# Kernel tuning notes

Measured on AMD Instinct MI355X. Metric: run time of the kernel, lower is better.

Reference implementation:

```python
import jax, jax.numpy as jnp
import numpy as np

B, T, E, H, V = 4, 2048, 1024, 16, 32000
HD = E // H  # head_dim = 64


def setup_inputs() -> dict:
    key = jax.random.key(0)
    ks = jax.random.split(key, 16)
    s = 0.02
    p = lambda k, shp: jax.random.normal(k, shp, jnp.float32) * s
    return {
        "x": jax.random.randint(ks[0], (B, T), 0, V),
        "tok_emb": p(ks[1], (V, E)),
        "pos_emb": p(ks[2], (T, E)),
        "m_Wq": p(ks[3], (E, E)), "m_Wk": p(ks[4], (E, E)),
        "m_Wv": p(ks[5], (E, E)), "m_Wo": p(ks[6], (E, E)),
        "m_bo": jnp.zeros((E,), jnp.float32),
        "h_Wq": p(ks[7], (E, E)), "h_Wk": p(ks[8], (E, E)),
        "h_Wv": p(ks[9], (E, E)), "h_Wo": p(ks[10], (E, E)),
        "h_bo": jnp.zeros((E,), jnp.float32),
        "f_W1": p(ks[11], (E, 512)), "f_b1": jnp.zeros((512,), jnp.float32),
        "f_W2": p(ks[12], (512, 1024)), "f_b2": jnp.zeros((1024,), jnp.float32),
        "f_W3": p(ks[13], (1024, 512)), "f_b3": jnp.zeros((512,), jnp.float32),
        "f_W4": p(ks[14], (512, E)), "f_b4": jnp.zeros((E,), jnp.float32),
        "ln_g": jnp.ones((E,), jnp.float32),
        "ln_b": jnp.zeros((E,), jnp.float32),
    }


def _layernorm(x, g, b, eps=1e-5):
    m = x.mean(-1, keepdims=True)
    v = ((x - m) ** 2).mean(-1, keepdims=True)
    return (x - m) / jnp.sqrt(v + eps) * g + b


def _mha(x, Wq, Wk, Wv, Wo, bo, masked):
    b, t, e = x.shape
    # [b, t, e] -> [b, h, t, hd]
    q = (x @ Wq).reshape(b, t, H, HD).transpose(0, 2, 1, 3)
    k = (x @ Wk).reshape(b, t, H, HD).transpose(0, 2, 1, 3)
    v = (x @ Wv).reshape(b, t, H, HD).transpose(0, 2, 1, 3)
    wei = jnp.einsum("bhqd,bhkd->bhqk", q, k) / np.float32(np.sqrt(HD))
    if masked:  # causal (module is in training mode by default)
        causal = jnp.tril(jnp.ones((t, t), dtype=bool))
        wei = jnp.where(causal, wei, -jnp.inf)
    att = jax.nn.softmax(wei, axis=-1)
    out = jnp.einsum("bhqk,bhkd->bhqd", att, v).transpose(0, 2, 1, 3).reshape(b, t, e)
    return out @ Wo + bo


def _ffn(x, W1, b1, W2, b2, W3, b3, W4, b4):
    h = jax.nn.relu(x @ W1 + b1)
    h = jax.nn.relu(h @ W2 + b2)
    h = jax.nn.relu(h @ W3 + b3)
    return h @ W4 + b4


def reference(x, tok_emb, pos_emb,
              m_Wq, m_Wk, m_Wv, m_Wo, m_bo,
              h_Wq, h_Wk, h_Wv, h_Wo, h_bo,
              f_W1, f_b1, f_W2, f_b2, f_W3, f_b3, f_W4, f_b4,
              ln_g, ln_b):
    e = tok_emb[x] + pos_emb[jnp.arange(x.shape[1])]          # [B, T, E]
    r = _layernorm(e + _mha(e, m_Wq, m_Wk, m_Wv, m_Wo, m_bo, True), ln_g, ln_b)
    r = _layernorm(r + _mha(r, h_Wq, h_Wk, h_Wv, h_Wo, h_bo, False), ln_g, ln_b)
    r = _layernorm(r + _ffn(r, f_W1, f_b1, f_W2, f_b2, f_W3, f_b3, f_W4, f_b4), ln_g, ln_b)
    return r
```

## Files before the change

kernel.cpp:

```cpp
#include <hip/hip_runtime.h>
#include <hip/hip_bf16.h>


typedef __attribute__((ext_vector_type(8))) short v8s;
typedef __attribute__((ext_vector_type(4))) short v4s;
typedef __attribute__((ext_vector_type(4))) float v4f;
typedef __attribute__((ext_vector_type(4))) unsigned int v4u;

#define MFMA16(a, b, c) __builtin_amdgcn_mfma_f32_16x16x32_bf16((a), (b), (c), 0, 0, 0)

typedef const __attribute__((address_space(1))) void* gas1_t;
typedef __attribute__((address_space(3))) void* las3_t;

__device__ __forceinline__ void gl_lds16(const void* g, void* l) {
  __builtin_amdgcn_global_load_lds((gas1_t)g, (las3_t)l, 16, 0, 0);
}

__device__ __forceinline__ unsigned short f2bf(float f) {
  __hip_bfloat16 h = __float2bfloat16(f);
  return *reinterpret_cast<unsigned short*>(&h);
}

__device__ __forceinline__ float bf2f(unsigned short u) {
  union { unsigned int i; float f; } v;
  v.i = (unsigned int)u << 16;
  return v.f;
}

__device__ __forceinline__ float fast_exp2(float x) {
  float r;
  asm("v_exp_f32 %0, %1" : "=v"(r) : "v"(x));
  return r;
}

__device__ __forceinline__ unsigned int cvt_pk_bf16(float lo, float hi) {
  unsigned int r;
  asm("v_cvt_pk_bf16_f32 %0, %1, %2" : "=v"(r) : "v"(lo), "v"(hi));
  return r;
}

__device__ __forceinline__ float max3f(float a, float b, float c) {
  float r;
  asm("v_max3_f32 %0, %1, %2, %3" : "=v"(r) : "v"(a), "v"(b), "v"(c));
  return r;
}

#define QSCALE 0.18033688011112042f

__global__ __launch_bounds__(256)
void transpose_bf16(const float* __restrict__ src, unsigned short* __restrict__ dst,
                    int K, int N) {
  __shared__ float tile[32][33];
  const int n0 = blockIdx.x * 32, k0 = blockIdx.y * 32;
  const int tx = threadIdx.x & 31, ty = threadIdx.x >> 5;
#pragma unroll
  for (int i = 0; i < 32; i += 8)
    tile[ty + i][tx] = src[(size_t)(k0 + ty + i) * N + n0 + tx];
  __syncthreads();
#pragma unroll
  for (int i = 0; i < 32; i += 8)
    dst[(size_t)(n0 + ty + i) * K + k0 + tx] = f2bf(tile[tx][ty + i]);
}

__global__ __launch_bounds__(256)
void embed_k(const int* __restrict__ x, const float* __restrict__ tok,
             const float* __restrict__ pos, unsigned short* __restrict__ act) {
  const int t = blockIdx.x, tid = threadIdx.x;
  const int id = x[t], tp = t & 2047;
  float4 v = ((const float4*)(tok + (size_t)id * 1024))[tid];
  float4 p = ((const float4*)(pos + (size_t)tp * 1024))[tid];
  ushort4 u;
  u.x = f2bf(v.x + p.x); u.y = f2bf(v.y + p.y);
  u.z = f2bf(v.z + p.z); u.w = f2bf(v.w + p.w);
  ((ushort4*)(act + (size_t)t * 1024))[tid] = u;
}

__global__ __launch_bounds__(256)
void gemm_bt(const unsigned short* __restrict__ A, const unsigned short* __restrict__ Bt,
             const float* __restrict__ bias, void* __restrict__ C,
             int M, int N, int K, int flags) {
  __shared__ __align__(16) unsigned short As[128 * 64];
  __shared__ __align__(16) unsigned short Bs[128 * 64];
  const int tid = threadIdx.x;
  const int w = tid >> 6, l = tid & 63;
  const int lr = l & 15, lg = l >> 4;
  const int wm = w & 1, wn = w >> 1;
  const int m0 = blockIdx.x * 128, n0 = blockIdx.y * 128;
  const int ra = l >> 3, ka = (l & 7) * 8;

  v4f acc[4][4];
  const v4f vzero = {0.f, 0.f, 0.f, 0.f};
#pragma unroll
  for (int m = 0; m < 4; ++m)
#pragma unroll
    for (int n = 0; n < 4; ++n) acc[m][n] = vzero;

  for (int k0 = 0; k0 < K; k0 += 64) {
#pragma unroll
    for (int i = 0; i < 4; ++i) {
      const int c = w + i * 4;
      gl_lds16(A  + (size_t)(m0 + c * 8 + ra) * K + k0 + ka, &As[c * 512]);
      gl_lds16(Bt + (size_t)(n0 + c * 8 + ra) * K + k0 + ka, &Bs[c * 512]);
    }
    __syncthreads();
#pragma unroll
    for (int kk = 0; kk < 2; ++kk) {
      v8s af[4], bb[4];
#pragma unroll
      for (int m = 0; m < 4; ++m)
        af[m] = *(const v8s*)&As[(wm * 64 + m * 16 + lr) * 64 + kk * 32 + lg * 8];
#pragma unroll
      for (int n = 0; n < 4; ++n)
        bb[n] = *(const v8s*)&Bs[(wn * 64 + n * 16 + lr) * 64 + kk * 32 + lg * 8];
#pragma unroll
      for (int m = 0; m < 4; ++m)
#pragma unroll
        for (int n = 0; n < 4; ++n)
          acc[m][n] = MFMA16(af[m], bb[n], acc[m][n]);
    }
    __syncthreads();
  }

  const bool relu = flags & 1, obf = flags & 2, qs = flags & 4;
#pragma unroll
  for (int n = 0; n < 4; ++n) {
    const int col = n0 + wn * 64 + n * 16 + lr;
    const float bv = bias ? bias[col] : 0.f;
    const float sc = (qs && col < 1024) ? QSCALE : 1.f;
#pragma unroll
    for (int m = 0; m < 4; ++m) {
      const int row = m0 + wm * 64 + m * 16 + lg * 4;
#pragma unroll
      for (int r = 0; r < 4; ++r) {
        float v = (acc[m][n][r] + bv) * sc;
        if (relu) v = fmaxf(v, 0.f);
        if (obf) ((unsigned short*)C)[(size_t)(row + r) * N + col] = f2bf(v);
        else     ((float*)C)[(size_t)(row + r) * N + col] = v;
      }
    }
  }
}

#define LDQ 3072
template <bool CAUSAL>
__global__ __launch_bounds__(512)
void flash_attn(const unsigned short* __restrict__ qkv, unsigned short* __restrict__ O) {
  __shared__ __align__(16) unsigned short Kt[64 * 64];
  __shared__ __align__(16) unsigned short Vt[64 * 64];
  const int tid = threadIdx.x;
  const int w = tid >> 6, l = tid & 63, lr = l & 15, lg = l >> 4;
  const int b = blockIdx.y >> 4, h = blockIdx.y & 15;
  const size_t baseq = ((size_t)b * 2048) * LDQ + h * 64;
  const size_t baseo = ((size_t)b * 2048) * 1024 + h * 64;
  const int kswz = (lr & 7) * 8;
  const int vswz = lr * 4;

  const int kra = l >> 3, kka = ((l & 7) ^ (l >> 3)) * 8;
  const int vp_ = tid & 31, vd0 = ((tid >> 5) & 7) * 8;

  const int nq = CAUSAL ? 2 : 1;
  for (int qi = 0; qi < nq; ++qi) {
    const int qt = CAUSAL ? (qi ? 15 - (int)blockIdx.x : (int)blockIdx.x)
                          : (int)blockIdx.x;
    const int q0w = qt * 128 + w * 16;

    const unsigned short* qp = qkv + baseq + (size_t)(q0w + lr) * LDQ + lg * 8;
    const v8s qf0 = *(const v8s*)qp;
    const v8s qf1 = *(const v8s*)(qp + 32);

    v4f acc[4];
    const v4f vzero = {0.f, 0.f, 0.f, 0.f};
#pragma unroll
    for (int n = 0; n < 4; ++n) acc[n] = vzero;
    float mrow = -INFINITY, lrow = 0.f;

    const int kv_end = CAUSAL ? qt * 128 + 128 : 2048;
    for (int kv0 = 0; kv0 < kv_end; kv0 += 64) {
      if (w >= 4) {
#pragma unroll
        for (int i = 0; i < 2; ++i) {
          const int c = (w - 4) * 2 + i;
          gl_lds16(qkv + baseq + 1024 + (size_t)(kv0 + c * 8 + kra) * LDQ + kka,
                   &Kt[c * 512]);
        }
      } else {
        const unsigned short* va = qkv + baseq + 2048 + (size_t)(kv0 + 2 * vp_) * LDQ + vd0;
        const v8s v0 = *(const v8s*)va;
        const v8s v1 = *(const v8s*)(va + LDQ);
#pragma unroll
        for (int j = 0; j < 8; ++j) {
          const unsigned int pk = (unsigned int)(unsigned short)v0[j] |
                                  ((unsigned int)(unsigned short)v1[j] << 16);
          *(unsigned int*)&Vt[(vd0 + j) * 64 + ((2 * vp_) ^ (((vd0 + j) & 15) * 4))] = pk;
        }
      }
      __syncthreads();

      v4f s[4];
#pragma unroll
      for (int n = 0; n < 4; ++n) s[n] = vzero;
      __builtin_amdgcn_s_setprio(1);
#pragma unroll
      for (int kk = 0; kk < 2; ++kk) {
#pragma unroll
        for (int n = 0; n < 4; ++n) {
          const v8s kf = *(const v8s*)&Kt[(n * 16 + lr) * 64 + ((kk * 32 + lg * 8) ^ kswz)];
          s[n] = MFMA16(kf, kk ? qf1 : qf0, s[n]);
        }
      }
      __builtin_amdgcn_s_setprio(0);

      if (CAUSAL && (kv0 + 63 > q0w)) {
        const int qg = q0w + lr;
#pragma unroll
        for (int n = 0; n < 4; ++n) {
          const int kvb = kv0 + n * 16 + lg * 4;
#pragma unroll
          for (int r = 0; r < 4; ++r)
            if (kvb + r > qg) s[n][r] = -INFINITY;
        }
      }

      float tm;
      {
        const float t0 = max3f(s[0][0], s[0][1], s[0][2]);
        const float t1 = max3f(s[0][3], s[1][0], s[1][1]);
        const float t2 = max3f(s[1][2], s[1][3], s[2][0]);
        const float t3 = max3f(s[2][1], s[2][2], s[2][3]);
        const float t4 = max3f(s[3][0], s[3][1], s[3][2]);
        tm = max3f(t0, t1, s[3][3]);
        tm = max3f(tm, t2, t3);
        tm = fmaxf(tm, t4);
      }
      tm = fmaxf(tm, __shfl_xor(tm, 16));
      tm = fmaxf(tm, __shfl_xor(tm, 32));

      if (__any(tm > mrow + 8.f)) {
        const float mn = fmaxf(mrow, tm);
        const float fac = fast_exp2(mrow - mn);
        mrow = mn;
        lrow *= fac;
        float facT[4];
#pragma unroll
        for (int r = 0; r < 4; ++r)
          facT[r] = __shfl(fac, (l & 48) | (lg * 4 + r));
#pragma unroll
        for (int n = 0; n < 4; ++n)
#pragma unroll
          for (int r = 0; r < 4; ++r) acc[n][r] *= facT[r];
      }

      float rs = 0.f;
#pragma unroll
      for (int n = 0; n < 4; ++n)
#pragma unroll
        for (int r = 0; r < 4; ++r) {
          s[n][r] = fast_exp2(s[n][r] - mrow);
          rs += s[n][r];
        }
      rs += __shfl_xor(rs, 16);
      rs += __shfl_xor(rs, 32);
      lrow += rs;

      v4u pu0, pu1;
      pu0.x = cvt_pk_bf16(s[0][0], s[0][1]); pu0.y = cvt_pk_bf16(s[0][2], s[0][3]);
      pu0.z = cvt_pk_bf16(s[1][0], s[1][1]); pu0.w = cvt_pk_bf16(s[1][2], s[1][3]);
      pu1.x = cvt_pk_bf16(s[2][0], s[2][1]); pu1.y = cvt_pk_bf16(s[2][2], s[2][3]);
      pu1.z = cvt_pk_bf16(s[3][0], s[3][1]); pu1.w = cvt_pk_bf16(s[3][2], s[3][3]);
      v8s pf0, pf1;
      __builtin_memcpy(&pf0, &pu0, 16);
      __builtin_memcpy(&pf1, &pu1, 16);

      __builtin_amdgcn_s_setprio(1);
#pragma unroll
      for (int kk = 0; kk < 2; ++kk) {
#pragma unroll
        for (int n = 0; n < 4; ++n) {
          const int rowb = (n * 16 + lr) * 64;
          const v4s va_ = *(const v4s*)&Vt[rowb + ((kk * 32 + lg * 4) ^ vswz)];
          const v4s vb_ = *(const v4s*)&Vt[rowb + ((kk * 32 + 16 + lg * 4) ^ vswz)];
          const v8s vf = __builtin_shufflevector(va_, vb_, 0, 1, 2, 3, 4, 5, 6, 7);
          acc[n] = MFMA16(kk ? pf1 : pf0, vf, acc[n]);
        }
      }
      __builtin_amdgcn_s_setprio(0);
      __syncthreads();
    }

    float lT[4];
#pragma unroll
    for (int r = 0; r < 4; ++r)
      lT[r] = __shfl(lrow, (l & 48) | (lg * 4 + r));
#pragma unroll
    for (int n = 0; n < 4; ++n)
#pragma unroll
      for (int r = 0; r < 4; ++r) {
        const float v = acc[n][r] / lT[r];
        O[baseo + (size_t)(q0w + lg * 4 + r) * 1024 + n * 16 + lr] = f2bf(v);
      }
  }
}

__global__ __launch_bounds__(256)
void add_ln(const unsigned short* __restrict__ ra, const unsigned short* __restrict__ rb,
            const float* __restrict__ g, const float* __restrict__ be,
            unsigned short* __restrict__ ob, float* __restrict__ of) {
  const int t = blockIdx.x, tid = threadIdx.x;
  const ushort4 ua = ((const ushort4*)(ra + (size_t)t * 1024))[tid];
  const ushort4 ub = ((const ushort4*)(rb + (size_t)t * 1024))[tid];
  float4 s;
  s.x = bf2f(ua.x) + bf2f(ub.x);
  s.y = bf2f(ua.y) + bf2f(ub.y);
  s.z = bf2f(ua.z) + bf2f(ub.z);
  s.w = bf2f(ua.w) + bf2f(ub.w);
  float sum = s.x + s.y + s.z + s.w;
  float sq  = s.x * s.x + s.y * s.y + s.z * s.z + s.w * s.w;
#pragma unroll
  for (int off = 32; off > 0; off >>= 1) {
    sum += __shfl_xor(sum, off);
    sq  += __shfl_xor(sq, off);
  }
  __shared__ float red[8];
  const int w = tid >> 6;
  if ((tid & 63) == 0) { red[w] = sum; red[4 + w] = sq; }
  __syncthreads();
  sum = red[0] + red[1] + red[2] + red[3];
  sq  = red[4] + red[5] + red[6] + red[7];
  const float mean = sum * (1.f / 1024.f);
  const float var  = sq * (1.f / 1024.f) - mean * mean;
  const float rstd = rsqrtf(var + 1e-5f);
  const float4 gg = ((const float4*)g)[tid];
  const float4 bb = ((const float4*)be)[tid];
  float4 y;
  y.x = (s.x - mean) * rstd * gg.x + bb.x;
  y.y = (s.y - mean) * rstd * gg.y + bb.y;
  y.z = (s.z - mean) * rstd * gg.z + bb.z;
  y.w = (s.w - mean) * rstd * gg.w + bb.w;
  if (ob) {
    ushort4 u;
    u.x = f2bf(y.x); u.y = f2bf(y.y); u.z = f2bf(y.z); u.w = f2bf(y.w);
    ((ushort4*)(ob + (size_t)t * 1024))[tid] = u;
  }
  if (of) ((float4*)(of + (size_t)t * 1024))[tid] = y;
}

extern "C" void kernel_launch(void* const* d_in, const int* in_sizes, int n_in,
                              void* d_out, int out_size, void* d_ws, size_t ws_size,
                              hipStream_t stream) {
  const int*   x    = (const int*)d_in[0];
  const float* tok  = (const float*)d_in[1];
  const float* pos  = (const float*)d_in[2];
  const float* mWq  = (const float*)d_in[3];
  const float* mWk  = (const float*)d_in[4];
  const float* mWv  = (const float*)d_in[5];
  const float* mWo  = (const float*)d_in[6];
  const float* m_bo = (const float*)d_in[7];
  const float* hWq  = (const float*)d_in[8];
  const float* hWk  = (const float*)d_in[9];
  const float* hWv  = (const float*)d_in[10];
  const float* hWo  = (const float*)d_in[11];
  const float* h_bo = (const float*)d_in[12];
  const float* fW1  = (const float*)d_in[13];
  const float* f_b1 = (const float*)d_in[14];
  const float* fW2  = (const float*)d_in[15];
  const float* f_b2 = (const float*)d_in[16];
  const float* fW3  = (const float*)d_in[17];
  const float* f_b3 = (const float*)d_in[18];
  const float* fW4  = (const float*)d_in[19];
  const float* f_b4 = (const float*)d_in[20];
  const float* ln_g = (const float*)d_in[21];
  const float* ln_b = (const float*)d_in[22];

  char* ws = (char*)d_ws;
  const size_t MB = 1ull << 20;
  unsigned short* wqkv1 = (unsigned short*)(ws + 0 * MB);
  unsigned short* wqkv2 = (unsigned short*)(ws + 6 * MB);
  unsigned short* wo1   = (unsigned short*)(ws + 12 * MB);
  unsigned short* wo2   = (unsigned short*)(ws + 14 * MB);
  unsigned short* fW1_t = (unsigned short*)(ws + 16 * MB);
  unsigned short* fW2_t = (unsigned short*)(ws + 17 * MB);
  unsigned short* fW3_t = (unsigned short*)(ws + 18 * MB);
  unsigned short* fW4_t = (unsigned short*)(ws + 19 * MB);
  unsigned short* actA  = (unsigned short*)(ws + 20 * MB);
  unsigned short* actB  = (unsigned short*)(ws + 36 * MB);
  unsigned short* tmp   = (unsigned short*)(ws + 52 * MB);
  unsigned short* qkv   = (unsigned short*)(ws + 68 * MB);
  unsigned short* h1    = (unsigned short*)(ws + 68 * MB);
  unsigned short* h2    = (unsigned short*)(ws + 76 * MB);
  unsigned short* h3    = (unsigned short*)(ws + 92 * MB);
  unsigned short* attno = (unsigned short*)(ws + 116 * MB);

  transpose_bf16<<<dim3(32, 32), 256, 0, stream>>>(mWq, wqkv1, 1024, 1024);
  transpose_bf16<<<dim3(32, 32), 256, 0, stream>>>(mWk, wqkv1 + 1024 * 1024, 1024, 1024);
  transpose_bf16<<<dim3(32, 32), 256, 0, stream>>>(mWv, wqkv1 + 2048 * 1024, 1024, 1024);
  transpose_bf16<<<dim3(32, 32), 256, 0, stream>>>(mWo, wo1, 1024, 1024);
  transpose_bf16<<<dim3(32, 32), 256, 0, stream>>>(hWq, wqkv2, 1024, 1024);
  transpose_bf16<<<dim3(32, 32), 256, 0, stream>>>(hWk, wqkv2 + 1024 * 1024, 1024, 1024);
  transpose_bf16<<<dim3(32, 32), 256, 0, stream>>>(hWv, wqkv2 + 2048 * 1024, 1024, 1024);
  transpose_bf16<<<dim3(32, 32), 256, 0, stream>>>(hWo, wo2, 1024, 1024);
  transpose_bf16<<<dim3(16, 32), 256, 0, stream>>>(fW1, fW1_t, 1024, 512);
  transpose_bf16<<<dim3(32, 16), 256, 0, stream>>>(fW2, fW2_t, 512, 1024);
  transpose_bf16<<<dim3(16, 32), 256, 0, stream>>>(fW3, fW3_t, 1024, 512);
  transpose_bf16<<<dim3(32, 16), 256, 0, stream>>>(fW4, fW4_t, 512, 1024);

  embed_k<<<8192, 256, 0, stream>>>(x, tok, pos, actA);

  gemm_bt<<<dim3(64, 24), 256, 0, stream>>>(actA, wqkv1, nullptr, qkv, 8192, 3072, 1024, 6);
  flash_attn<true><<<dim3(8, 64), 512, 0, stream>>>(qkv, attno);
  gemm_bt<<<dim3(64, 8), 256, 0, stream>>>(attno, wo1, m_bo, tmp, 8192, 1024, 1024, 2);
  add_ln<<<8192, 256, 0, stream>>>(actA, tmp, ln_g, ln_b, actB, nullptr);

  gemm_bt<<<dim3(64, 24), 256, 0, stream>>>(actB, wqkv2, nullptr, qkv, 8192, 3072, 1024, 6);
  flash_attn<false><<<dim3(16, 64), 512, 0, stream>>>(qkv, attno);
  gemm_bt<<<dim3(64, 8), 256, 0, stream>>>(attno, wo2, h_bo, tmp, 8192, 1024, 1024, 2);
  add_ln<<<8192, 256, 0, stream>>>(actB, tmp, ln_g, ln_b, actA, nullptr);

  gemm_bt<<<dim3(64, 4), 256, 0, stream>>>(actA, fW1_t, f_b1, h1, 8192, 512, 1024, 3);
  gemm_bt<<<dim3(64, 8), 256, 0, stream>>>(h1, fW2_t, f_b2, h2, 8192, 1024, 512, 3);
  gemm_bt<<<dim3(64, 4), 256, 0, stream>>>(h2, fW3_t, f_b3, h3, 8192, 512, 1024, 3);
  gemm_bt<<<dim3(64, 8), 256, 0, stream>>>(h3, fW4_t, f_b4, tmp, 8192, 1024, 512, 2);
  add_ln<<<8192, 256, 0, stream>>>(actA, tmp, ln_g, ln_b, nullptr, (float*)d_out);
}
```

Measured before the change: 581.6 us.

## Use 32x32 MFMA with swizzled LDS in GEMM and batch weight transposes

The GEMM inner loop moves from 16x16x32 MFMA tiles to 32x32x16 MFMA tiles, so each wave loads two A and two B fragments per k-step instead of four of each. An XOR swizzle is applied to the global-to-LDS load column and to the fragment reads, aimed at avoiding LDS bank conflicts. The twelve per-weight transpose launches are merged into one launch driven by a descriptor struct, which cuts launch overhead. The epilogue writes are reindexed for the 32x32 accumulator layout, with 16 scattered stores per lane.

```diff
diff --git a/kernel.cpp b/kernel.cpp
--- a/kernel.cpp
+++ b/kernel.cpp
@@ -5,9 +5,11 @@
 typedef __attribute__((ext_vector_type(8))) short v8s;
 typedef __attribute__((ext_vector_type(4))) short v4s;
 typedef __attribute__((ext_vector_type(4))) float v4f;
+typedef __attribute__((ext_vector_type(16))) float v16f;
 typedef __attribute__((ext_vector_type(4))) unsigned int v4u;
 
 #define MFMA16(a, b, c) __builtin_amdgcn_mfma_f32_16x16x32_bf16((a), (b), (c), 0, 0, 0)
+#define MFMA32(a, b, c) __builtin_amdgcn_mfma_f32_32x32x16_bf16((a), (b), (c), 0, 0, 0)
 
 typedef const __attribute__((address_space(1))) void* gas1_t;
 typedef __attribute__((address_space(3))) void* las3_t;
@@ -47,19 +49,35 @@
 
 #define QSCALE 0.18033688011112042f
 
+struct TransDesc {
+  const float* src[12];
+  unsigned short* dst[12];
+};
+
 __global__ __launch_bounds__(256)
-void transpose_bf16(const float* __restrict__ src, unsigned short* __restrict__ dst,
-                    int K, int N) {
-  __shared__ float tile[32][33];
-  const int n0 = blockIdx.x * 32, k0 = blockIdx.y * 32;
+void transpose_all(TransDesc td) {
+  const int bid = blockIdx.x;
+  int m, tile, K, N;
+  if (bid < 8192) { m = bid >> 10; tile = bid & 1023; K = 1024; N = 1024; }
+  else {
+    const int r = bid - 8192;
+    m = 8 + (r >> 9); tile = r & 511;
+    if (m & 1) { K = 512; N = 1024; } else { K = 1024; N = 512; }
+  }
+  const float* src = td.src[m];
+  unsigned short* dst = td.dst[m];
+  const int ntx = N >> 5;
+  const int n0 = (tile % ntx) * 32, k0 = (tile / ntx) * 32;
+
+  __shared__ float tile_s[32][33];
   const int tx = threadIdx.x & 31, ty = threadIdx.x >> 5;
 #pragma unroll
   for (int i = 0; i < 32; i += 8)
-    tile[ty + i][tx] = src[(size_t)(k0 + ty + i) * N + n0 + tx];
+    tile_s[ty + i][tx] = src[(size_t)(k0 + ty + i) * N + n0 + tx];
   __syncthreads();
 #pragma unroll
   for (int i = 0; i < 32; i += 8)
-    dst[(size_t)(n0 + ty + i) * K + k0 + tx] = f2bf(tile[tx][ty + i]);
+    dst[(size_t)(n0 + ty + i) * K + k0 + tx] = f2bf(tile_s[tx][ty + i]);
 }
 
 __global__ __launch_bounds__(256)
@@ -83,17 +101,19 @@
   __shared__ __align__(16) unsigned short Bs[128 * 64];
   const int tid = threadIdx.x;
   const int w = tid >> 6, l = tid & 63;
-  const int lr = l & 15, lg = l >> 4;
+  const int l31 = l & 31, l5 = l >> 5;
   const int wm = w & 1, wn = w >> 1;
   const int m0 = blockIdx.x * 128, n0 = blockIdx.y * 128;
-  const int ra = l >> 3, ka = (l & 7) * 8;
-
-  v4f acc[4][4];
-  const v4f vzero = {0.f, 0.f, 0.f, 0.f};
-#pragma unroll
-  for (int m = 0; m < 4; ++m)
-#pragma unroll
-    for (int n = 0; n < 4; ++n) acc[m][n] = vzero;
+  const int ra = l >> 3, ka = ((l & 7) ^ (l >> 3)) * 8;
+  const int fswz = (l31 & 7) * 8;
+
+  v16f acc[2][2];
+#pragma unroll
+  for (int bm = 0; bm < 2; ++bm)
+#pragma unroll
+    for (int bn = 0; bn < 2; ++bn)
+#pragma unroll
+      for (int r = 0; r < 16; ++r) acc[bm][bn][r] = 0.f;
 
   for (int k0 = 0; k0 < K; k0 += 64) {
 #pragma unroll
@@ -104,38 +124,36 @@
     }
     __syncthreads();
 #pragma unroll
-    for (int kk = 0; kk < 2; ++kk) {
-      v8s af[4], bb[4];
-#pragma unroll
-      for (int m = 0; m < 4; ++m)
-        af[m] = *(const v8s*)&As[(wm * 64 + m * 16 + lr) * 64 + kk * 32 + lg * 8];
-#pragma unroll
-      for (int n = 0; n < 4; ++n)
-        bb[n] = *(const v8s*)&Bs[(wn * 64 + n * 16 + lr) * 64 + kk * 32 + lg * 8];
-#pragma unroll
-      for (int m = 0; m < 4; ++m)
-#pragma unroll
-        for (int n = 0; n < 4; ++n)
-          acc[m][n] = MFMA16(af[m], bb[n], acc[m][n]);
+    for (int kk = 0; kk < 4; ++kk) {
+      const int co = (kk * 16 + l5 * 8) ^ fswz;
+      const v8s a0 = *(const v8s*)&As[(wm * 64 + l31) * 64 + co];
+      const v8s a1 = *(const v8s*)&As[(wm * 64 + 32 + l31) * 64 + co];
+      const v8s b0 = *(const v8s*)&Bs[(wn * 64 + l31) * 64 + co];
+      const v8s b1 = *(const v8s*)&Bs[(wn * 64 + 32 + l31) * 64 + co];
+      acc[0][0] = MFMA32(a0, b0, acc[0][0]);
+      acc[0][1] = MFMA32(a0, b1, acc[0][1]);
+      acc[1][0] = MFMA32(a1, b0, acc[1][0]);
+      acc[1][1] = MFMA32(a1, b1, acc[1][1]);
     }
     __syncthreads();
   }
 
   const bool relu = flags & 1, obf = flags & 2, qs = flags & 4;
 #pragma unroll
-  for (int n = 0; n < 4; ++n) {
-    const int col = n0 + wn * 64 + n * 16 + lr;
+  for (int bn = 0; bn < 2; ++bn) {
+    const int col = n0 + wn * 64 + bn * 32 + l31;
     const float bv = bias ? bias[col] : 0.f;
     const float sc = (qs && col < 1024) ? QSCALE : 1.f;
 #pragma unroll
-    for (int m = 0; m < 4; ++m) {
-      const int row = m0 + wm * 64 + m * 16 + lg * 4;
-#pragma unroll
-      for (int r = 0; r < 4; ++r) {
-        float v = (acc[m][n][r] + bv) * sc;
+    for (int bm = 0; bm < 2; ++bm) {
+      const int rowbase = m0 + wm * 64 + bm * 32 + 4 * l5;
+#pragma unroll
+      for (int r = 0; r < 16; ++r) {
+        const int row = rowbase + (r & 3) + 8 * (r >> 2);
+        float v = (acc[bm][bn][r] + bv) * sc;
         if (relu) v = fmaxf(v, 0.f);
-        if (obf) ((unsigned short*)C)[(size_t)(row + r) * N + col] = f2bf(v);
-        else     ((float*)C)[(size_t)(row + r) * N + col] = v;
+        if (obf) ((unsigned short*)C)[(size_t)row * N + col] = f2bf(v);
+        else     ((float*)C)[(size_t)row * N + col] = v;
       }
     }
   }
@@ -390,18 +408,20 @@
   unsigned short* h3    = (unsigned short*)(ws + 92 * MB);
   unsigned short* attno = (unsigned short*)(ws + 116 * MB);
 
-  transpose_bf16<<<dim3(32, 32), 256, 0, stream>>>(mWq, wqkv1, 1024, 1024);
-  transpose_bf16<<<dim3(32, 32), 256, 0, stream>>>(mWk, wqkv1 + 1024 * 1024, 1024, 1024);
-  transpose_bf16<<<dim3(32, 32), 256, 0, stream>>>(mWv, wqkv1 + 2048 * 1024, 1024, 1024);
-  transpose_bf16<<<dim3(32, 32), 256, 0, stream>>>(mWo, wo1, 1024, 1024);
-  transpose_bf16<<<dim3(32, 32), 256, 0, stream>>>(hWq, wqkv2, 1024, 1024);
-  transpose_bf16<<<dim3(32, 32), 256, 0, stream>>>(hWk, wqkv2 + 1024 * 1024, 1024, 1024);
-  transpose_bf16<<<dim3(32, 32), 256, 0, stream>>>(hWv, wqkv2 + 2048 * 1024, 1024, 1024);
-  transpose_bf16<<<dim3(32, 32), 256, 0, stream>>>(hWo, wo2, 1024, 1024);
-  transpose_bf16<<<dim3(16, 32), 256, 0, stream>>>(fW1, fW1_t, 1024, 512);
-  transpose_bf16<<<dim3(32, 16), 256, 0, stream>>>(fW2, fW2_t, 512, 1024);
-  transpose_bf16<<<dim3(16, 32), 256, 0, stream>>>(fW3, fW3_t, 1024, 512);
-  transpose_bf16<<<dim3(32, 16), 256, 0, stream>>>(fW4, fW4_t, 512, 1024);
+  TransDesc td;
+  td.src[0] = mWq; td.dst[0] = wqkv1;
+  td.src[1] = mWk; td.dst[1] = wqkv1 + 1024 * 1024;
+  td.src[2] = mWv; td.dst[2] = wqkv1 + 2048 * 1024;
+  td.src[3] = mWo; td.dst[3] = wo1;
+  td.src[4] = hWq; td.dst[4] = wqkv2;
+  td.src[5] = hWk; td.dst[5] = wqkv2 + 1024 * 1024;
+  td.src[6] = hWv; td.dst[6] = wqkv2 + 2048 * 1024;
+  td.src[7] = hWo; td.dst[7] = wo2;
+  td.src[8] = fW1; td.dst[8] = fW1_t;
+  td.src[9] = fW2; td.dst[9] = fW2_t;
+  td.src[10] = fW3; td.dst[10] = fW3_t;
+  td.src[11] = fW4; td.dst[11] = fW4_t;
+  transpose_all<<<10240, 256, 0, stream>>>(td);
 
   embed_k<<<8192, 256, 0, stream>>>(x, tok, pos, actA);
 
```

Result: faster. 504.1 us (-13.3%).
